# Kernel optimization log

Measured on AMD Instinct MI355X. Metric: run time of the kernel, lower is better.

## Reference

```python
import jax, jax.numpy as jnp
import numpy as np

N_ATOM, N_QUERY, KNN = 100000, 20000, 32
E = N_QUERY * KNN
HID, EDGE_F, HEADS = 128, 16, 8
D_HEAD = HID // HEADS
LN_EPS = 1e-5


def setup_inputs() -> dict:
    key = jax.random.key(0)
    ks = jax.random.split(key, 16)
    s = 1.0 / np.sqrt(HID)
    src = jax.random.randint(ks[0], (E,), 0, N_ATOM)
    dst = jnp.repeat(jnp.arange(N_QUERY), KNN)  # each query has KNN incoming edges
    return {
        "h_atom": jax.random.normal(ks[1], (N_ATOM, HID), jnp.float32),
        "h_query": jax.random.normal(ks[2], (N_QUERY, HID), jnp.float32),
        "edge_attr": jax.random.uniform(ks[3], (E, EDGE_F), jnp.float32),
        "W_q": jax.random.normal(ks[4], (HID, HID), jnp.float32) * s,
        "W_k": jax.random.normal(ks[5], (HID, HID), jnp.float32) * s,
        "W_v": jax.random.normal(ks[6], (HID, HID), jnp.float32) * s,
        "W_rbf": jax.random.normal(ks[7], (HEADS, EDGE_F), jnp.float32) * (1.0 / np.sqrt(EDGE_F)),
        "W1": jax.random.normal(ks[8], (HID, 2 * HID), jnp.float32) * (1.0 / np.sqrt(2 * HID)),
        "b1": jnp.zeros((HID,), jnp.float32),
        "W2": jax.random.normal(ks[9], (HID, HID), jnp.float32) * s,
        "b2": jnp.zeros((HID,), jnp.float32),
        "ln_gamma": jnp.ones((HID,), jnp.float32),
        "ln_beta": jnp.zeros((HID,), jnp.float32),
        "edge_index": jnp.stack([src, dst]),
        "n_query": N_QUERY,
    }


def reference(h_atom, h_query, edge_attr, W_q, W_k, W_v, W_rbf, W1, b1, W2, b2,
              ln_gamma, ln_beta, edge_index, n_query):
    src, dst = edge_index[0], edge_index[1]
    En = src.shape[0]
    # gather + project, per-edge multi-head Q/K/V  [E, H, d]
    Q = (h_query[dst] @ W_q.T).reshape(En, HEADS, D_HEAD)
    K = (h_atom[src] @ W_k.T).reshape(En, HEADS, D_HEAD)
    V = (h_atom[src] @ W_v.T).reshape(En, HEADS, D_HEAD)
    scores = jnp.einsum("ehd,ehd->eh", Q, K) / np.sqrt(D_HEAD) + edge_attr @ W_rbf.T  # [E,H]
    # segment softmax over edges sharing the same dst query, per head
    seg_max = jax.lax.stop_gradient(jax.ops.segment_max(scores, dst, num_segments=n_query))
    ex = jnp.exp(scores - seg_max[dst])
    denom = jax.ops.segment_sum(ex, dst, num_segments=n_query)
    alpha = ex / (denom[dst] + 1e-16)  # [E,H]
    # weighted scatter-add aggregation
    msgs = (alpha[:, :, None] * V).reshape(En, HID)
    agg = jax.ops.segment_sum(msgs, dst, num_segments=n_query)  # [Nq, HID]
    # update MLP + residual + LayerNorm
    z = jnp.concatenate([h_query, agg], axis=-1)
    delta = jax.nn.relu(z @ W1.T + b1) @ W2.T + b2
    y = h_query + delta
    mu = y.mean(-1, keepdims=True)
    var = y.var(-1, keepdims=True)
    return (y - mu) / jnp.sqrt(var + LN_EPS) * ln_gamma + ln_beta
```

## Files before the change

kernel.cpp:

```cpp
#include <hip/hip_runtime.h>
#include <hip/hip_bf16.h>
#include <math.h>

#define N_ATOM   100000
#define N_QUERY  20000
#define KNN      32
#define EDGES    (N_QUERY * KNN)

typedef __attribute__((ext_vector_type(8))) short  short8;
typedef __attribute__((ext_vector_type(4))) float  floatx4;
typedef __attribute__((ext_vector_type(2))) float  fx2;

static __device__ __forceinline__ unsigned short f2bf_bits(float f) {
  union { __hip_bfloat16 h; unsigned short u; } cv;
  cv.h = __float2bfloat16(f);
  return cv.u;
}
static __device__ __forceinline__ float bflo(unsigned int u) { return __uint_as_float(u << 16); }
static __device__ __forceinline__ float bfhi(unsigned int u) { return __uint_as_float(u & 0xffff0000u); }

__global__ void pack_all_kernel(const float* __restrict__ Wq, const float* __restrict__ Wk,
                                const float* __restrict__ Wv, const float* __restrict__ W1,
                                const float* __restrict__ W2,
                                const float* __restrict__ edge_attr, const float* __restrict__ Wrbf,
                                unsigned short* __restrict__ WKVp, unsigned short* __restrict__ WQp,
                                unsigned short* __restrict__ W1p,  unsigned short* __restrict__ W2p,
                                float* __restrict__ ED) {
  int tid = blockIdx.x * blockDim.x + threadIdx.x;
  if (tid < 98304) {
    const float *Wa, *Wb; int nsplit, Kd, Nd; unsigned short* dst; float scale = 1.0f;
    int t = tid;
    if (t < 32768)      { Wa = Wk; Wb = Wv; nsplit = 128; Kd = 128; Nd = 256; dst = WKVp; }
    else if (t < 49152) { t -= 32768; Wa = Wq; Wb = Wq; nsplit = 128; Kd = 128; Nd = 128; dst = WQp; scale = 0.25f; }
    else if (t < 81920) { t -= 49152; Wa = W1; Wb = W1; nsplit = 128; Kd = 256; Nd = 128; dst = W1p; }
    else                { t -= 81920; Wa = W2; Wb = W2; nsplit = 128; Kd = 128; Nd = 128; dst = W2p; }
    int j    = t & 7;
    int lane = (t >> 3) & 63;
    int t2   = t >> 9;
    int NT   = Nd >> 4;
    int ntile = t2 % NT;
    int ktile = t2 / NT;
    int k = ktile * 32 + (lane >> 4) * 8 + j;
    int n = ntile * 16 + (lane & 15);
    float v = (n < nsplit) ? Wa[(size_t)n * Kd + k] : Wb[(size_t)(n - nsplit) * Kd + k];
    dst[t] = f2bf_bits(v * scale);
  } else {
    int e = tid - 98304;
    if (e >= EDGES) return;
    const float4* ea = (const float4*)(edge_attr + (size_t)e * 16);
    float4 x0 = ea[0], x1 = ea[1], x2 = ea[2], x3 = ea[3];
    float4 r0, r1;
#pragma unroll
    for (int h = 0; h < 8; h++) {
      const float4* wp = (const float4*)(Wrbf + h * 16);
      float4 w0 = wp[0], w1 = wp[1], w2 = wp[2], w3 = wp[3];
      float d = w0.x*x0.x + w0.y*x0.y + w0.z*x0.z + w0.w*x0.w
              + w1.x*x1.x + w1.y*x1.y + w1.z*x1.z + w1.w*x1.w
              + w2.x*x2.x + w2.y*x2.y + w2.z*x2.z + w2.w*x2.w
              + w3.x*x3.x + w3.y*x3.y + w3.z*x3.z + w3.w*x3.w;
      if (h < 4) ((float*)&r0)[h] = d; else ((float*)&r1)[h - 4] = d;
    }
    float4* dst = (float4*)(ED + (size_t)e * 8);
    dst[0] = r0; dst[1] = r1;
  }
}

__global__ __launch_bounds__(256, 2) void gemm_kvq(
    const float* __restrict__ h_atom, const float* __restrict__ h_query,
    const unsigned short* __restrict__ WKVp, const unsigned short* __restrict__ WQp,
    unsigned char* __restrict__ Kp8, unsigned char* __restrict__ Vp8,
    unsigned short* __restrict__ Qb) {
  constexpr int KVGROUPS = (N_ATOM + 63) / 64;
  constexpr int QGROUPS  = (N_QUERY + 63) / 64;
  constexpr int KVB = 464;
  __shared__ unsigned short Wlds[32768];
  const int tid  = threadIdx.x;
  const int l    = tid & 63;
  const int w    = tid >> 6;
  const int quad = l >> 4;
  const int col0 = l & 15;
  const int woff = w * 16 + col0;
  const bool isKV = (int)blockIdx.x < KVB;

  if (isKV) {
    const uint4* gsrc = (const uint4*)WKVp;
    uint4* ldst = (uint4*)Wlds;
#pragma unroll
    for (int it = 0; it < 16; it++) ldst[it * 256 + tid] = gsrc[it * 256 + tid];
  } else {
    const uint4* gsrc = (const uint4*)WQp;
    uint4* ldst = (uint4*)Wlds;
#pragma unroll
    for (int it = 0; it < 8; it++) ldst[it * 256 + tid] = gsrc[it * 256 + tid];
  }

  if (isKV) {
    int g = (int)blockIdx.x;
    floatx4 a[8];
    {
      int r = g * 64 + woff; if (r >= N_ATOM) r = N_ATOM - 1;
      const float* ap = h_atom + (size_t)r * 128 + quad * 8;
#pragma unroll
      for (int k0 = 0; k0 < 4; k0++) {
        a[2*k0]   = *(const floatx4*)(ap + k0 * 32);
        a[2*k0+1] = *(const floatx4*)(ap + k0 * 32 + 4);
      }
    }
    __syncthreads();

    for (; g < KVGROUPS; g += KVB) {
      const int gn = g + KVB;
      floatx4 an[8];
#pragma unroll
      for (int i = 0; i < 8; i++) an[i] = (floatx4){0.f, 0.f, 0.f, 0.f};
      if (gn < KVGROUPS) {
        int r = gn * 64 + woff; if (r >= N_ATOM) r = N_ATOM - 1;
        const float* ap = h_atom + (size_t)r * 128 + quad * 8;
#pragma unroll
        for (int k0 = 0; k0 < 4; k0++) {
          an[2*k0]   = *(const floatx4*)(ap + k0 * 32);
          an[2*k0+1] = *(const floatx4*)(ap + k0 * 32 + 4);
        }
      }
      __builtin_amdgcn_sched_barrier(0);

      short8 af[4];
#pragma unroll
      for (int k0 = 0; k0 < 4; k0++) {
        af[k0][0] = (short)f2bf_bits(a[2*k0][0]);   af[k0][1] = (short)f2bf_bits(a[2*k0][1]);
        af[k0][2] = (short)f2bf_bits(a[2*k0][2]);   af[k0][3] = (short)f2bf_bits(a[2*k0][3]);
        af[k0][4] = (short)f2bf_bits(a[2*k0+1][0]); af[k0][5] = (short)f2bf_bits(a[2*k0+1][1]);
        af[k0][6] = (short)f2bf_bits(a[2*k0+1][2]); af[k0][7] = (short)f2bf_bits(a[2*k0+1][3]);
      }

      floatx4 acc[16];
#pragma unroll
      for (int i = 0; i < 16; i++) acc[i] = (floatx4){0.f, 0.f, 0.f, 0.f};
#pragma unroll
      for (int k0 = 0; k0 < 4; k0++) {
        const unsigned short* bbase = Wlds + k0 * 8192 + l * 8;
#pragma unroll
        for (int nt = 0; nt < 16; nt++) {
          short8 bf = *(const short8*)(bbase + nt * 512);
          acc[nt] = __builtin_amdgcn_mfma_f32_16x16x32_bf16(bf, af[k0], acc[nt], 0, 0, 0);
        }
      }

      const int grow = g * 64 + woff;
      if (grow < N_ATOM) {
        unsigned char* kbase = Kp8 + (size_t)grow * 128 + quad * 4;
        unsigned char* vbase = Vp8 + (size_t)grow * 128 + quad * 4;
#pragma unroll
        for (int nt = 0; nt < 16; nt++) {
          int pk = __builtin_amdgcn_cvt_pk_fp8_f32(acc[nt][0], acc[nt][1], 0, false);
          pk     = __builtin_amdgcn_cvt_pk_fp8_f32(acc[nt][2], acc[nt][3], pk, true);
          if (nt < 8) *(int*)(kbase + nt * 16) = pk;
          else        *(int*)(vbase + (nt - 8) * 16) = pk;
        }
      }

#pragma unroll
      for (int i = 0; i < 8; i++) a[i] = an[i];
    }
  } else {
    int g = (int)blockIdx.x - KVB;
    floatx4 a[8];
    {
      int r = g * 64 + woff; if (r >= N_QUERY) r = N_QUERY - 1;
      const float* ap = h_query + (size_t)r * 128 + quad * 8;
#pragma unroll
      for (int k0 = 0; k0 < 4; k0++) {
        a[2*k0]   = *(const floatx4*)(ap + k0 * 32);
        a[2*k0+1] = *(const floatx4*)(ap + k0 * 32 + 4);
      }
    }
    __syncthreads();

    for (; g < QGROUPS; g += 512 - KVB) {
      const int gn = g + (512 - KVB);
      floatx4 an[8];
#pragma unroll
      for (int i = 0; i < 8; i++) an[i] = (floatx4){0.f, 0.f, 0.f, 0.f};
      if (gn < QGROUPS) {
        int r = gn * 64 + woff; if (r >= N_QUERY) r = N_QUERY - 1;
        const float* ap = h_query + (size_t)r * 128 + quad * 8;
#pragma unroll
        for (int k0 = 0; k0 < 4; k0++) {
          an[2*k0]   = *(const floatx4*)(ap + k0 * 32);
          an[2*k0+1] = *(const floatx4*)(ap + k0 * 32 + 4);
        }
      }
      __builtin_amdgcn_sched_barrier(0);

      short8 af[4];
#pragma unroll
      for (int k0 = 0; k0 < 4; k0++) {
        af[k0][0] = (short)f2bf_bits(a[2*k0][0]);   af[k0][1] = (short)f2bf_bits(a[2*k0][1]);
        af[k0][2] = (short)f2bf_bits(a[2*k0][2]);   af[k0][3] = (short)f2bf_bits(a[2*k0][3]);
        af[k0][4] = (short)f2bf_bits(a[2*k0+1][0]); af[k0][5] = (short)f2bf_bits(a[2*k0+1][1]);
        af[k0][6] = (short)f2bf_bits(a[2*k0+1][2]); af[k0][7] = (short)f2bf_bits(a[2*k0+1][3]);
      }

      floatx4 acc[8];
#pragma unroll
      for (int i = 0; i < 8; i++) acc[i] = (floatx4){0.f, 0.f, 0.f, 0.f};
#pragma unroll
      for (int k0 = 0; k0 < 4; k0++) {
        const unsigned short* bbase = Wlds + k0 * 4096 + l * 8;
#pragma unroll
        for (int nt = 0; nt < 8; nt++) {
          short8 bf = *(const short8*)(bbase + nt * 512);
          acc[nt] = __builtin_amdgcn_mfma_f32_16x16x32_bf16(bf, af[k0], acc[nt], 0, 0, 0);
        }
      }

      const int grow = g * 64 + woff;
      if (grow < N_QUERY) {
#pragma unroll
        for (int nt = 0; nt < 8; nt++) {
          unsigned u0 = (unsigned)f2bf_bits(acc[nt][0]) | ((unsigned)f2bf_bits(acc[nt][1]) << 16);
          unsigned u1 = (unsigned)f2bf_bits(acc[nt][2]) | ((unsigned)f2bf_bits(acc[nt][3]) << 16);
          uint2 uu; uu.x = u0; uu.y = u1;
          *(uint2*)(Qb + (size_t)grow * 128 + nt * 16 + quad * 4) = uu;
        }
      }

#pragma unroll
      for (int i = 0; i < 8; i++) a[i] = an[i];
    }
  }
}

__global__ __launch_bounds__(256, 4) void attn_kernel(
    const unsigned short* __restrict__ Qb,
    const unsigned char* __restrict__ Kp8,
    const unsigned char* __restrict__ Vp8,
    const float* __restrict__ ED,
    const int* __restrict__ src,
    float* __restrict__ Agg) {
  const int l = threadIdx.x & 63;
  const int w = threadIdx.x >> 6;
  const int q = blockIdx.x * 4 + w;
  const int j = l >> 3;
  const int h = l & 7;
  const int e0 = q * KNN;

  int s0 = src[e0 +  0 + j];
  int s1 = src[e0 +  8 + j];
  int s2 = src[e0 + 16 + j];
  int s3 = src[e0 + 24 + j];

  const float* edp = ED + (size_t)e0 * 8 + l;
  float ed0 = edp[0];
  float ed1 = edp[64];
  float ed2 = edp[128];
  float ed3 = edp[192];

  const uint4* qp = (const uint4*)(Qb + (size_t)q * 128 + h * 16);
  uint4 qA = qp[0], qB = qp[1];

  uint4 kq0 = *(const uint4*)(Kp8 + (size_t)s0 * 128 + h * 16);
  uint4 kq1 = *(const uint4*)(Kp8 + (size_t)s1 * 128 + h * 16);
  uint4 kq2 = *(const uint4*)(Kp8 + (size_t)s2 * 128 + h * 16);
  uint4 kq3 = *(const uint4*)(Kp8 + (size_t)s3 * 128 + h * 16);
  uint4 vq0 = *(const uint4*)(Vp8 + (size_t)s0 * 128 + h * 16);
  uint4 vq1 = *(const uint4*)(Vp8 + (size_t)s1 * 128 + h * 16);
  uint4 vq2 = *(const uint4*)(Vp8 + (size_t)s2 * 128 + h * 16);
  uint4 vq3 = *(const uint4*)(Vp8 + (size_t)s3 * 128 + h * 16);

  float qd[16];
  qd[0]  = bflo(qA.x); qd[1]  = bfhi(qA.x); qd[2]  = bflo(qA.y); qd[3]  = bfhi(qA.y);
  qd[4]  = bflo(qA.z); qd[5]  = bfhi(qA.z); qd[6]  = bflo(qA.w); qd[7]  = bfhi(qA.w);
  qd[8]  = bflo(qB.x); qd[9]  = bfhi(qB.x); qd[10] = bflo(qB.y); qd[11] = bfhi(qB.y);
  qd[12] = bflo(qB.z); qd[13] = bfhi(qB.z); qd[14] = bflo(qB.w); qd[15] = bfhi(qB.w);

  float acc[16];
#pragma unroll
  for (int i = 0; i < 16; i++) acc[i] = 0.f;
  float lsum = 0.f;

  auto dopass = [&](const uint4& kq, const uint4& vq, float ed) {
    float kd = 0.f;
    {
      fx2 f0, f1;
      f0 = __builtin_amdgcn_cvt_pk_f32_fp8((int)kq.x, false);
      f1 = __builtin_amdgcn_cvt_pk_f32_fp8((int)kq.x, true);
      kd += qd[0] * f0[0] + qd[1] * f0[1] + qd[2] * f1[0] + qd[3] * f1[1];
      f0 = __builtin_amdgcn_cvt_pk_f32_fp8((int)kq.y, false);
      f1 = __builtin_amdgcn_cvt_pk_f32_fp8((int)kq.y, true);
      kd += qd[4] * f0[0] + qd[5] * f0[1] + qd[6] * f1[0] + qd[7] * f1[1];
      f0 = __builtin_amdgcn_cvt_pk_f32_fp8((int)kq.z, false);
      f1 = __builtin_amdgcn_cvt_pk_f32_fp8((int)kq.z, true);
      kd += qd[8] * f0[0] + qd[9] * f0[1] + qd[10] * f1[0] + qd[11] * f1[1];
      f0 = __builtin_amdgcn_cvt_pk_f32_fp8((int)kq.w, false);
      f1 = __builtin_amdgcn_cvt_pk_f32_fp8((int)kq.w, true);
      kd += qd[12] * f0[0] + qd[13] * f0[1] + qd[14] * f1[0] + qd[15] * f1[1];
    }
    float pe = __expf(kd + ed);
    lsum += pe;
    {
      fx2 g0, g1;
      g0 = __builtin_amdgcn_cvt_pk_f32_fp8((int)vq.x, false);
      g1 = __builtin_amdgcn_cvt_pk_f32_fp8((int)vq.x, true);
      acc[0] += pe * g0[0]; acc[1] += pe * g0[1]; acc[2] += pe * g1[0]; acc[3] += pe * g1[1];
      g0 = __builtin_amdgcn_cvt_pk_f32_fp8((int)vq.y, false);
      g1 = __builtin_amdgcn_cvt_pk_f32_fp8((int)vq.y, true);
      acc[4] += pe * g0[0]; acc[5] += pe * g0[1]; acc[6] += pe * g1[0]; acc[7] += pe * g1[1];
      g0 = __builtin_amdgcn_cvt_pk_f32_fp8((int)vq.z, false);
      g1 = __builtin_amdgcn_cvt_pk_f32_fp8((int)vq.z, true);
      acc[8] += pe * g0[0]; acc[9] += pe * g0[1]; acc[10] += pe * g1[0]; acc[11] += pe * g1[1];
      g0 = __builtin_amdgcn_cvt_pk_f32_fp8((int)vq.w, false);
      g1 = __builtin_amdgcn_cvt_pk_f32_fp8((int)vq.w, true);
      acc[12] += pe * g0[0]; acc[13] += pe * g0[1]; acc[14] += pe * g1[0]; acc[15] += pe * g1[1];
    }
  };
  dopass(kq0, vq0, ed0);
  dopass(kq1, vq1, ed1);
  dopass(kq2, vq2, ed2);
  dopass(kq3, vq3, ed3);

  lsum += __shfl_xor(lsum, 8, 64);
  lsum += __shfl_xor(lsum, 16, 64);
  lsum += __shfl_xor(lsum, 32, 64);

  float r8[8];
  const bool hiA = (l & 32) != 0;
#pragma unroll
  for (int i = 0; i < 8; i++) {
    float keep = hiA ? acc[i + 8] : acc[i];
    float send = hiA ? acc[i]     : acc[i + 8];
    r8[i] = keep + __shfl_xor(send, 32, 64);
  }
  float r4[4];
  const bool hiB = (l & 16) != 0;
#pragma unroll
  for (int i = 0; i < 4; i++) {
    float keep = hiB ? r8[i + 4] : r8[i];
    float send = hiB ? r8[i]     : r8[i + 4];
    r4[i] = keep + __shfl_xor(send, 16, 64);
  }
  float r2[2];
  const bool hiC = (l & 8) != 0;
#pragma unroll
  for (int i = 0; i < 2; i++) {
    float keep = hiC ? r4[i + 2] : r4[i];
    float send = hiC ? r4[i]     : r4[i + 2];
    r2[i] = keep + __shfl_xor(send, 8, 64);
  }
  float inv = 1.f / (lsum + 1e-16f);
  float2 o; o.x = r2[0] * inv; o.y = r2[1] * inv;
  *(float2*)(Agg + (size_t)q * 128 + h * 16 + 2 * j) = o;
}

__global__ __launch_bounds__(256, 1) void mlp_kernel(
    const float* __restrict__ h_query, const float* __restrict__ Agg,
    const unsigned short* __restrict__ W1p, const unsigned short* __restrict__ W2p,
    const float* __restrict__ b1, const float* __restrict__ b2,
    const float* __restrict__ gamma, const float* __restrict__ beta,
    float* __restrict__ out) {
  constexpr int M = N_QUERY;
  constexpr int STRIDE = 136;
  __shared__ unsigned short Wlds[16384];
  __shared__ unsigned short hid[64 * STRIDE];

  const int tid  = threadIdx.x;
  const int l    = tid & 63;
  const int w    = tid >> 6;
  const int quad = l >> 4;
  const int col0 = l & 15;
  const int row0 = blockIdx.x * 64 + w * 16;
  const int grow = row0 + col0;
  const int arow = grow < M ? grow : M - 1;

  const float* hp = h_query + (size_t)arow * 128 + quad * 8;
  const float* gp = Agg     + (size_t)arow * 128 + quad * 8;
  floatx4 a[16];
#pragma unroll
  for (int k0 = 0; k0 < 4; k0++) {
    a[2*k0]       = *(const floatx4*)(hp + k0 * 32);
    a[2*k0+1]     = *(const floatx4*)(hp + k0 * 32 + 4);
    a[8 + 2*k0]   = *(const floatx4*)(gp + k0 * 32);
    a[8 + 2*k0+1] = *(const floatx4*)(gp + k0 * 32 + 4);
  }

  {
    const uint4* gsrc = (const uint4*)W1p;
    uint4* ldst = (uint4*)Wlds;
#pragma unroll
    for (int it = 0; it < 8; it++) ldst[it * 256 + tid] = gsrc[it * 256 + tid];
  }

  short8 af[8];
#pragma unroll
  for (int t = 0; t < 8; t++) {
    af[t][0] = (short)f2bf_bits(a[2*t][0]);   af[t][1] = (short)f2bf_bits(a[2*t][1]);
    af[t][2] = (short)f2bf_bits(a[2*t][2]);   af[t][3] = (short)f2bf_bits(a[2*t][3]);
    af[t][4] = (short)f2bf_bits(a[2*t+1][0]); af[t][5] = (short)f2bf_bits(a[2*t+1][1]);
    af[t][6] = (short)f2bf_bits(a[2*t+1][2]); af[t][7] = (short)f2bf_bits(a[2*t+1][3]);
  }
  __syncthreads();

  floatx4 acc[8];
#pragma unroll
  for (int i = 0; i < 8; i++) acc[i] = (floatx4){0.f, 0.f, 0.f, 0.f};
#pragma unroll
  for (int kt = 0; kt < 4; kt++) {
    const unsigned short* bbase = Wlds + kt * 4096 + l * 8;
#pragma unroll
    for (int nt = 0; nt < 8; nt++) {
      short8 bf = *(const short8*)(bbase + nt * 512);
      acc[nt] = __builtin_amdgcn_mfma_f32_16x16x32_bf16(bf, af[kt], acc[nt], 0, 0, 0);
    }
  }
  __syncthreads();

  {
    const uint4* gsrc = (const uint4*)(W1p + 16384);
    uint4* ldst = (uint4*)Wlds;
#pragma unroll
    for (int it = 0; it < 8; it++) ldst[it * 256 + tid] = gsrc[it * 256 + tid];
  }
  __syncthreads();

#pragma unroll
  for (int kt = 0; kt < 4; kt++) {
    const unsigned short* bbase = Wlds + kt * 4096 + l * 8;
#pragma unroll
    for (int nt = 0; nt < 8; nt++) {
      short8 bf = *(const short8*)(bbase + nt * 512);
      acc[nt] = __builtin_amdgcn_mfma_f32_16x16x32_bf16(bf, af[4 + kt], acc[nt], 0, 0, 0);
    }
  }

  {
    const int rl = w * 16 + col0;
#pragma unroll
    for (int nt = 0; nt < 8; nt++) {
      const int c = nt * 16 + quad * 4;
      float4 bb = *(const float4*)(b1 + c);
      unsigned u0 = (unsigned)f2bf_bits(fmaxf(acc[nt][0] + bb.x, 0.f))
                  | ((unsigned)f2bf_bits(fmaxf(acc[nt][1] + bb.y, 0.f)) << 16);
      unsigned u1 = (unsigned)f2bf_bits(fmaxf(acc[nt][2] + bb.z, 0.f))
                  | ((unsigned)f2bf_bits(fmaxf(acc[nt][3] + bb.w, 0.f)) << 16);
      uint2 uu; uu.x = u0; uu.y = u1;
      *(uint2*)(hid + rl * STRIDE + c) = uu;
    }
  }
  __syncthreads();

  {
    const uint4* gsrc = (const uint4*)W2p;
    uint4* ldst = (uint4*)Wlds;
#pragma unroll
    for (int it = 0; it < 8; it++) ldst[it * 256 + tid] = gsrc[it * 256 + tid];
  }
  __syncthreads();

  floatx4 acc2[8];
#pragma unroll
  for (int i = 0; i < 8; i++) acc2[i] = (floatx4){0.f, 0.f, 0.f, 0.f};
  const int rloc = w * 16 + col0;
#pragma unroll
  for (int k0 = 0; k0 < 128; k0 += 32) {
    short8 af2 = *(const short8*)(hid + rloc * STRIDE + k0 + quad * 8);
    const unsigned short* bbase = Wlds + (k0 >> 5) * 4096 + l * 8;
#pragma unroll
    for (int nt = 0; nt < 8; nt++) {
      short8 bf = *(const short8*)(bbase + nt * 512);
      acc2[nt] = __builtin_amdgcn_mfma_f32_16x16x32_bf16(bf, af2, acc2[nt], 0, 0, 0);
    }
  }

  const int rr = grow < M ? grow : M - 1;
  float v[8][4];
  float s1 = 0.f, s2 = 0.f;
#pragma unroll
  for (int nt = 0; nt < 8; nt++) {
    const int c = nt * 16 + quad * 4;
    float4 hq = *(const float4*)(h_query + (size_t)rr * 128 + c);
    float4 bb = *(const float4*)(b2 + c);
    float t0 = acc2[nt][0] + bb.x + hq.x;
    float t1 = acc2[nt][1] + bb.y + hq.y;
    float t2 = acc2[nt][2] + bb.z + hq.z;
    float t3 = acc2[nt][3] + bb.w + hq.w;
    v[nt][0] = t0; v[nt][1] = t1; v[nt][2] = t2; v[nt][3] = t3;
    s1 += t0 + t1 + t2 + t3;
    s2 += t0 * t0 + t1 * t1 + t2 * t2 + t3 * t3;
  }
  s1 += __shfl_xor(s1, 16, 64); s1 += __shfl_xor(s1, 32, 64);
  s2 += __shfl_xor(s2, 16, 64); s2 += __shfl_xor(s2, 32, 64);
  float mean = s1 * (1.0f / 128.0f);
  float var  = s2 * (1.0f / 128.0f) - mean * mean;
  float rstd = rsqrtf(var + 1e-5f);
  if (grow < M) {
#pragma unroll
    for (int nt = 0; nt < 8; nt++) {
      const int c = nt * 16 + quad * 4;
      float4 gg = *(const float4*)(gamma + c);
      float4 be = *(const float4*)(beta + c);
      float4 o;
      o.x = (v[nt][0] - mean) * rstd * gg.x + be.x;
      o.y = (v[nt][1] - mean) * rstd * gg.y + be.y;
      o.z = (v[nt][2] - mean) * rstd * gg.z + be.z;
      o.w = (v[nt][3] - mean) * rstd * gg.w + be.w;
      *(float4*)(out + (size_t)grow * 128 + c) = o;
    }
  }
}

extern "C" void kernel_launch(void* const* d_in, const int* in_sizes, int n_in,
                              void* d_out, int out_size, void* d_ws, size_t ws_size,
                              hipStream_t stream) {
  const float* h_atom    = (const float*)d_in[0];
  const float* h_query   = (const float*)d_in[1];
  const float* edge_attr = (const float*)d_in[2];
  const float* W_q  = (const float*)d_in[3];
  const float* W_k  = (const float*)d_in[4];
  const float* W_v  = (const float*)d_in[5];
  const float* Wrbf = (const float*)d_in[6];
  const float* W1   = (const float*)d_in[7];
  const float* b1   = (const float*)d_in[8];
  const float* W2   = (const float*)d_in[9];
  const float* b2   = (const float*)d_in[10];
  const float* ln_g = (const float*)d_in[11];
  const float* ln_b = (const float*)d_in[12];
  const int* edge_index = (const int*)d_in[13];
  float* out = (float*)d_out;

  char* ws = (char*)d_ws;
  unsigned char*  Kp8 = (unsigned char*)(ws);
  unsigned char*  Vp8 = (unsigned char*)(ws + 12800000);
  unsigned short* Qb  = (unsigned short*)(ws + 25600000);
  float* Agg          = (float*)(ws + 30720000);
  unsigned short* WKVp = (unsigned short*)(ws + 40960000);
  unsigned short* WQp  = WKVp + 32768;
  unsigned short* W1p  = WQp  + 16384;
  unsigned short* W2p  = W1p  + 32768;
  float* ED           = (float*)(ws + 41160704);

  pack_all_kernel<<<(98304 + EDGES + 255) / 256, 256, 0, stream>>>(
      W_q, W_k, W_v, W1, W2, edge_attr, Wrbf, WKVp, WQp, W1p, W2p, ED);

  gemm_kvq<<<512, 256, 0, stream>>>(h_atom, h_query, WKVp, WQp, Kp8, Vp8, Qb);

  attn_kernel<<<N_QUERY / 4, 256, 0, stream>>>(Qb, Kp8, Vp8, ED, edge_index, Agg);

  mlp_kernel<<<(N_QUERY + 63) / 64, 256, 0, stream>>>(
      h_query, Agg, W1p, W2p, b1, b2, ln_g, ln_b, out);
}
```

Measured before the change: 214.5 us.

## Split K and V projection into separate blocks to halve LDS and raise occupancy

The fused KV projection blocks are split into separate K blocks and V blocks, each loading only its half of the packed weight into LDS (32KB instead of 64KB) and keeping 8 accumulators instead of 16. The grid doubles to 1024 blocks, the launch bound asks for 4 blocks per CU, and the Q part gets 96 blocks. The aim is more resident waves to hide h_atom load latency. In exchange, each h_atom row is now read and converted to bf16 twice, once by a K block and once by a V block.

New measurement: 217.4 us. About the same (+1.3%).

```diff
diff --git a/kernel.cpp b/kernel.cpp
--- a/kernel.cpp
+++ b/kernel.cpp
@@ -65,37 +65,37 @@
   }
 }
 
-__global__ __launch_bounds__(256, 2) void gemm_kvq(
+__global__ __launch_bounds__(256, 4) void gemm_kvq(
     const float* __restrict__ h_atom, const float* __restrict__ h_query,
     const unsigned short* __restrict__ WKVp, const unsigned short* __restrict__ WQp,
     unsigned char* __restrict__ Kp8, unsigned char* __restrict__ Vp8,
     unsigned short* __restrict__ Qb) {
   constexpr int KVGROUPS = (N_ATOM + 63) / 64;
   constexpr int QGROUPS  = (N_QUERY + 63) / 64;
-  constexpr int KVB = 464;
-  __shared__ unsigned short Wlds[32768];
+  constexpr int NKB = 464, NVB = 464, NQB = 96;
+  __shared__ unsigned short Wlds[16384];
   const int tid  = threadIdx.x;
   const int l    = tid & 63;
   const int w    = tid >> 6;
   const int quad = l >> 4;
   const int col0 = l & 15;
   const int woff = w * 16 + col0;
-  const bool isKV = (int)blockIdx.x < KVB;
-
-  if (isKV) {
-    const uint4* gsrc = (const uint4*)WKVp;
-    uint4* ldst = (uint4*)Wlds;
-#pragma unroll
-    for (int it = 0; it < 16; it++) ldst[it * 256 + tid] = gsrc[it * 256 + tid];
-  } else {
-    const uint4* gsrc = (const uint4*)WQp;
-    uint4* ldst = (uint4*)Wlds;
-#pragma unroll
-    for (int it = 0; it < 8; it++) ldst[it * 256 + tid] = gsrc[it * 256 + tid];
-  }
-
-  if (isKV) {
-    int g = (int)blockIdx.x;
+  const int bid  = (int)blockIdx.x;
+
+  if (bid < NKB + NVB) {
+    const bool isV = bid >= NKB;
+    {
+      const uint4* gsrc = (const uint4*)WKVp;
+      uint4* ldst = (uint4*)Wlds;
+      const int voff = isV ? 512 : 0;
+#pragma unroll
+      for (int it = 0; it < 8; it++) {
+        int idx = it * 256 + tid;
+        int kt = idx >> 9, wi = idx & 511;
+        ldst[idx] = gsrc[kt * 1024 + voff + wi];
+      }
+    }
+    int g = isV ? bid - NKB : bid;
     floatx4 a[8];
     {
       int r = g * 64 + woff; if (r >= N_ATOM) r = N_ATOM - 1;
@@ -108,8 +108,9 @@
     }
     __syncthreads();
 
-    for (; g < KVGROUPS; g += KVB) {
-      const int gn = g + KVB;
+    unsigned char* Op8 = isV ? Vp8 : Kp8;
+    for (; g < KVGROUPS; g += NKB) {
+      const int gn = g + NKB;
       floatx4 an[8];
 #pragma unroll
       for (int i = 0; i < 8; i++) an[i] = (floatx4){0.f, 0.f, 0.f, 0.f};
@@ -133,14 +134,14 @@
         af[k0][6] = (short)f2bf_bits(a[2*k0+1][2]); af[k0][7] = (short)f2bf_bits(a[2*k0+1][3]);
       }
 
-      floatx4 acc[16];
-#pragma unroll
-      for (int i = 0; i < 16; i++) acc[i] = (floatx4){0.f, 0.f, 0.f, 0.f};
+      floatx4 acc[8];
+#pragma unroll
+      for (int i = 0; i < 8; i++) acc[i] = (floatx4){0.f, 0.f, 0.f, 0.f};
 #pragma unroll
       for (int k0 = 0; k0 < 4; k0++) {
-        const unsigned short* bbase = Wlds + k0 * 8192 + l * 8;
-#pragma unroll
-        for (int nt = 0; nt < 16; nt++) {
+        const unsigned short* bbase = Wlds + k0 * 4096 + l * 8;
+#pragma unroll
+        for (int nt = 0; nt < 8; nt++) {
           short8 bf = *(const short8*)(bbase + nt * 512);
           acc[nt] = __builtin_amdgcn_mfma_f32_16x16x32_bf16(bf, af[k0], acc[nt], 0, 0, 0);
         }
@@ -148,14 +149,12 @@
 
       const int grow = g * 64 + woff;
       if (grow < N_ATOM) {
-        unsigned char* kbase = Kp8 + (size_t)grow * 128 + quad * 4;
-        unsigned char* vbase = Vp8 + (size_t)grow * 128 + quad * 4;
-#pragma unroll
-        for (int nt = 0; nt < 16; nt++) {
+        unsigned char* obase = Op8 + (size_t)grow * 128 + quad * 4;
+#pragma unroll
+        for (int nt = 0; nt < 8; nt++) {
           int pk = __builtin_amdgcn_cvt_pk_fp8_f32(acc[nt][0], acc[nt][1], 0, false);
           pk     = __builtin_amdgcn_cvt_pk_fp8_f32(acc[nt][2], acc[nt][3], pk, true);
-          if (nt < 8) *(int*)(kbase + nt * 16) = pk;
-          else        *(int*)(vbase + (nt - 8) * 16) = pk;
+          *(int*)(obase + nt * 16) = pk;
         }
       }
 
@@ -163,7 +162,13 @@
       for (int i = 0; i < 8; i++) a[i] = an[i];
     }
   } else {
-    int g = (int)blockIdx.x - KVB;
+    {
+      const uint4* gsrc = (const uint4*)WQp;
+      uint4* ldst = (uint4*)Wlds;
+#pragma unroll
+      for (int it = 0; it < 8; it++) ldst[it * 256 + tid] = gsrc[it * 256 + tid];
+    }
+    int g = bid - (NKB + NVB);
     floatx4 a[8];
     {
       int r = g * 64 + woff; if (r >= N_QUERY) r = N_QUERY - 1;
@@ -176,8 +181,8 @@
     }
     __syncthreads();
 
-    for (; g < QGROUPS; g += 512 - KVB) {
-      const int gn = g + (512 - KVB);
+    for (; g < QGROUPS; g += NQB) {
+      const int gn = g + NQB;
       floatx4 an[8];
 #pragma unroll
       for (int i = 0; i < 8; i++) an[i] = (floatx4){0.f, 0.f, 0.f, 0.f};
@@ -541,7 +546,7 @@
   pack_all_kernel<<<(98304 + EDGES + 255) / 256, 256, 0, stream>>>(
       W_q, W_k, W_v, W1, W2, edge_attr, Wrbf, WKVp, WQp, W1p, W2p, ED);
 
-  gemm_kvq<<<512, 256, 0, stream>>>(h_atom, h_query, WKVp, WQp, Kp8, Vp8, Qb);
+  gemm_kvq<<<1024, 256, 0, stream>>>(h_atom, h_query, WKVp, WQp, Kp8, Vp8, Qb);
 
   attn_kernel<<<N_QUERY / 4, 256, 0, stream>>>(Qb, Kp8, Vp8, ED, edge_index, Agg);
 
```
